# Optimization experiments

Hardware: AMD Instinct MI355X
Metric: run time of the kernel (lower is better)

The kernel has to match this reference:

```python
import jax, jax.numpy as jnp
import numpy as np

INPUT, HIDDEN = 40, 250
B, T = 256, 512


def lstm_layer(x_seq, W_ih, W_hh, b_ih, b_hh):
    """x_seq: [B,T,D_in] -> [B,T,H]. PyTorch gate order: i,f,g,o."""
    # Precompute input contribution with one big GEMM: [B,T,4H]
    xg = jnp.einsum('btd,gd->btg', x_seq, W_ih) + b_ih + b_hh
    xg_t = jnp.transpose(xg, (1, 0, 2))  # [T,B,4H]
    H = W_hh.shape[1]
    h0 = jnp.zeros((x_seq.shape[0], H), dtype=x_seq.dtype)
    c0 = jnp.zeros_like(h0)

    def step(carry, g_in):
        h, c = carry
        g = g_in + h @ W_hh.T  # [B,4H]
        i = jax.nn.sigmoid(g[:, :H])
        f = jax.nn.sigmoid(g[:, H:2 * H])
        gg = jnp.tanh(g[:, 2 * H:3 * H])
        o = jax.nn.sigmoid(g[:, 3 * H:])
        c = f * c + i * gg
        h = o * jnp.tanh(c)
        return (h, c), h

    _, hs = jax.lax.scan(step, (h0, c0), xg_t)  # hs: [T,B,H]
    return jnp.transpose(hs, (1, 0, 2))


def setup_inputs() -> dict:
    key = jax.random.key(0)
    ks = jax.random.split(key, 12)
    s_in = 1.0 / np.sqrt(HIDDEN)  # PyTorch LSTM init scale
    u = lambda k, shape: jax.random.uniform(k, shape, jnp.float32, -s_in, s_in)
    return {
        'x': jax.random.normal(ks[0], (B, T, INPUT), jnp.float32),
        'W_ih0': u(ks[1], (4 * HIDDEN, INPUT)),
        'W_hh0': u(ks[2], (4 * HIDDEN, HIDDEN)),
        'b_ih0': u(ks[3], (4 * HIDDEN,)),
        'b_hh0': u(ks[4], (4 * HIDDEN,)),
        'W_ih1': u(ks[5], (4 * HIDDEN, HIDDEN)),
        'W_hh1': u(ks[6], (4 * HIDDEN, HIDDEN)),
        'b_ih1': u(ks[7], (4 * HIDDEN,)),
        'b_hh1': u(ks[8], (4 * HIDDEN,)),
        'W_lin': u(ks[9], (1, HIDDEN)),
        'b_lin': u(ks[10], (1,)),
    }


def reference(x, W_ih0, W_hh0, b_ih0, b_hh0, W_ih1, W_hh1, b_ih1, b_hh1, W_lin, b_lin):
    h1 = lstm_layer(x, W_ih0, W_hh0, b_ih0, b_hh0)   # [B,T,H]
    h2 = lstm_layer(h1, W_ih1, W_hh1, b_ih1, b_hh1)  # [B,T,H]
    y = jnp.einsum('bth,oh->bto', h2, W_lin) + b_lin  # [B,T,1]
    return jax.nn.sigmoid(y)
```

## Files before the change

kernel.cpp:

```cpp
#include <hip/hip_runtime.h>
#include <cstdint>

#define B_TOT 256
#define T_LEN 512
#define NX    40
#define NH    250
#define HP    256
#define XP    64
#define K0    (XP + HP)
#define K1    (HP + HP)
#define MB    32
#define NU    16
#define NR    64
#define RING  8
#define LDSK  520
#define SLOTS 16
#define NFLAG (2 * 8 * 16 * SLOTS)
#define RSTEP (B_TOT * HP / 2)
#define XCD_AT(w) ((w) * SLOTS + 8)
#define BAR_IDX 9
#define GETREG_XCC 63508

typedef __attribute__((ext_vector_type(8))) short short8;
typedef __attribute__((ext_vector_type(4))) float float4v;

__device__ __forceinline__ unsigned short f2bf(float f) {
  unsigned u = __float_as_uint(f);
  u += 0x7FFFu + ((u >> 16) & 1u);
  return (unsigned short)(u >> 16);
}
__device__ __forceinline__ float bf2f(unsigned short h) {
  return __uint_as_float(((unsigned)h) << 16);
}
__device__ __forceinline__ float sigm(float x) { return 1.0f / (1.0f + __expf(-x)); }
__device__ __forceinline__ float tanh_f(float x) {
  float e = __expf(-2.0f * fabsf(x));
  float t = (1.0f - e) / (1.0f + e);
  return copysignf(t, x);
}
__device__ __forceinline__ unsigned ld_lic(const unsigned* p) {
  return __hip_atomic_load(p, __ATOMIC_RELAXED, __HIP_MEMORY_SCOPE_AGENT);
}
__device__ __forceinline__ void inv_l1() {
  asm volatile("buffer_inv\n\ts_waitcnt vmcnt(0)" ::: "memory");
  __builtin_amdgcn_sched_barrier(0);
}
template <bool FAST>
__device__ __forceinline__ unsigned ldh(const unsigned* p) {
  if (FAST) return *p;
  return ld_lic(p);
}
template <bool FAST>
__device__ __forceinline__ void sth(unsigned* p, unsigned v) {
  if (FAST) *p = v;
  else __hip_atomic_store(p, v, __ATOMIC_RELAXED, __HIP_MEMORY_SCOPE_AGENT);
}

template <int KSTEPS, int LAYER, bool FAST>
__device__ __forceinline__ void run_layer(
    int tid, int gg, int b0, int u0,
    const float* __restrict__ x, float* __restrict__ out, float blinv,
    unsigned short* __restrict__ h1bc, unsigned short* __restrict__ h2bc,
    int* __restrict__ c0s, int* __restrict__ c1s, int* __restrict__ mys,
    unsigned short (*WL)[LDSK], unsigned short (*inA)[LDSK],
    float (*gbuf)[NR + 4], float* biasS, float* wlinS) {
  const int lane = tid & 63, wv = tid >> 6;
  const int quad = lane >> 4, l15 = lane & 15;
  const int Mt = wv & 1, Np = wv >> 1;
  const int gb = b0 >> 5;
  const int irow = tid >> 3, icol = tid & 7;

  short8 bfrag[2][KSTEPS];
#pragma unroll
  for (int ks = 0; ks < KSTEPS; ++ks) {
#pragma unroll
    for (int i = 0; i < 2; ++i)
      bfrag[i][ks] = *(const short8*)&WL[Np * 32 + i * 16 + l15][ks * 32 + quad * 8];
  }

  float cA = 0.f, cB = 0.f;

#pragma unroll 1
  for (int t = 0; t < T_LEN; ++t) {
    if (wv == 0 && lane < 32) {
      const int* sl = ((lane < 16) ? c0s : c1s) + (lane & 15) * SLOTS;
      int thr;
      if (LAYER == 0) thr = (lane < 16) ? t : (t - RING + 1);
      else            thr = (lane < 16) ? (t + 1) : t;
      while (__hip_atomic_load(sl, __ATOMIC_RELAXED, __HIP_MEMORY_SCOPE_AGENT) < thr) {
        __builtin_amdgcn_s_sleep(1);
      }
    }
    __syncthreads();
    if (FAST && (LAYER == 1 || t > 0)) inv_l1();

    if (LAYER == 0) {
      if (t > 0) {
        const unsigned* s1 = (const unsigned*)h1bc +
            ((size_t)((t - 1) & (RING - 1)) * RSTEP + (size_t)gb * 4096);
        unsigned v[16];
#pragma unroll
        for (int k = 0; k < 16; ++k) v[k] = ldh<FAST>(s1 + tid + k * 256);
#pragma unroll
        for (int k = 0; k < 16; ++k)
          ((unsigned*)&inA[irow][0])[32 + k * 8 + icol] = v[k];
      }
      if (tid < 128) {
        int b = tid >> 2, c = tid & 3;
        const float* xp = x + ((size_t)(b0 + b) * T_LEN + (size_t)t) * NX + c * 10;
#pragma unroll
        for (int j = 0; j < 10; ++j) inA[b][c * 10 + j] = f2bf(xp[j]);
      }
    } else {
      const unsigned* s1 = (const unsigned*)h1bc +
          ((size_t)(t & (RING - 1)) * RSTEP + (size_t)gb * 4096);
      unsigned va[16], vb[16];
#pragma unroll
      for (int k = 0; k < 16; ++k) va[k] = ldh<FAST>(s1 + tid + k * 256);
      if (t > 0) {
        const unsigned* s2 = (const unsigned*)h2bc +
            ((size_t)((t - 1) & (RING - 1)) * RSTEP + (size_t)gb * 4096);
#pragma unroll
        for (int k = 0; k < 16; ++k) vb[k] = ldh<FAST>(s2 + tid + k * 256);
      }
#pragma unroll
      for (int k = 0; k < 16; ++k) {
        unsigned* row = (unsigned*)&inA[irow][0];
        row[k * 8 + icol] = va[k];
        if (t > 0) row[128 + k * 8 + icol] = vb[k];
      }
    }
    __syncthreads();

    float4v acc0 = {0.f, 0.f, 0.f, 0.f};
    float4v acc1 = {0.f, 0.f, 0.f, 0.f};
#pragma unroll
    for (int ks = 0; ks < KSTEPS; ++ks) {
      short8 a = *(const short8*)&inA[Mt * 16 + l15][ks * 32 + quad * 8];
      acc0 = __builtin_amdgcn_mfma_f32_16x16x32_bf16(a, bfrag[0][ks], acc0, 0, 0, 0);
      acc1 = __builtin_amdgcn_mfma_f32_16x16x32_bf16(a, bfrag[1][ks], acc1, 0, 0, 0);
    }
#pragma unroll
    for (int reg = 0; reg < 4; ++reg) {
      gbuf[Mt * 16 + quad * 4 + reg][Np * 32 + l15] = acc0[reg];
      gbuf[Mt * 16 + quad * 4 + reg][Np * 32 + 16 + l15] = acc1[reg];
    }
    __syncthreads();

    {
      int eb = tid >> 3, up = tid & 7;
      float4v ga = *(const float4v*)&gbuf[eb][up * 8];
      float4v gv = *(const float4v*)&gbuf[eb][up * 8 + 4];
      float iA = sigm(ga[0] + biasS[up * 8 + 0]);
      float fA = sigm(ga[1] + biasS[up * 8 + 1]);
      float gA = tanh_f(ga[2] + biasS[up * 8 + 2]);
      float oA = sigm(ga[3] + biasS[up * 8 + 3]);
      cA = fA * cA + iA * gA;
      float hA = oA * tanh_f(cA);
      float iB = sigm(gv[0] + biasS[up * 8 + 4]);
      float fB = sigm(gv[1] + biasS[up * 8 + 5]);
      float gB = tanh_f(gv[2] + biasS[up * 8 + 6]);
      float oB = sigm(gv[3] + biasS[up * 8 + 7]);
      cB = fB * cB + iB * gB;
      float hB = oB * tanh_f(cB);
      unsigned hv = (unsigned)f2bf(hA) | ((unsigned)f2bf(hB) << 16);
      unsigned* dst = (unsigned*)(LAYER ? h2bc : h1bc);
      size_t di = (size_t)(t & (RING - 1)) * RSTEP + (size_t)gb * 4096 +
                  (size_t)gg * 256 + tid;
      sth<FAST>(dst + di, hv);
    }

    __syncthreads();
    if (tid == 0)
      sth<FAST>((unsigned*)mys, (unsigned)(t + 1));

    if (LAYER == 1 && gg == 0 && t > 0) {
      int eb = tid >> 3, uc = tid & 7;
      float sum = 0.f;
#pragma unroll
      for (int j = 0; j < 4; ++j) {
        short8 hvv = *(const short8*)&inA[eb][HP + uc * 32 + j * 8];
#pragma unroll
        for (int e = 0; e < 8; ++e)
          sum += bf2f((unsigned short)hvv[e]) * wlinS[uc * 32 + j * 8 + e];
      }
      sum += __shfl_xor(sum, 1);
      sum += __shfl_xor(sum, 2);
      sum += __shfl_xor(sum, 4);
      if ((tid & 7) == 0)
        out[(size_t)(b0 + eb) * T_LEN + (t - 1)] = sigm(sum + blinv);
    }
  }

  if (LAYER == 1 && gg == 0) {
    if (wv == 0 && lane < 16) {
      const int* sl = c1s + lane * SLOTS;
      while (__hip_atomic_load(sl, __ATOMIC_RELAXED, __HIP_MEMORY_SCOPE_AGENT) < T_LEN) {
        __builtin_amdgcn_s_sleep(1);
      }
    }
    __syncthreads();
    if (FAST) inv_l1();
    int eb = tid >> 3, uc = tid & 7;
    const unsigned* base = (const unsigned*)h2bc +
        ((size_t)(511 & (RING - 1)) * RSTEP + (size_t)gb * 4096);
    float sum = 0.f;
#pragma unroll
    for (int g = 0; g < 2; ++g) {
      const unsigned* src = base + (size_t)(2 * uc + g) * 256 + eb * 8;
#pragma unroll
      for (int j = 0; j < 8; ++j) {
        unsigned dw = ldh<FAST>(src + j);
        sum += bf2f((unsigned short)(dw & 0xFFFFu)) * wlinS[uc * 32 + g * 16 + 2 * j];
        sum += bf2f((unsigned short)(dw >> 16)) * wlinS[uc * 32 + g * 16 + 2 * j + 1];
      }
    }
    sum += __shfl_xor(sum, 1);
    sum += __shfl_xor(sum, 2);
    sum += __shfl_xor(sum, 4);
    if ((tid & 7) == 0)
      out[(size_t)(b0 + eb) * T_LEN + 511] = sigm(sum + blinv);
  }
}

extern "C" __global__ void __launch_bounds__(256, 1) lstm_persist(
    const float* __restrict__ x,
    const float* __restrict__ Wih0, const float* __restrict__ Whh0,
    const float* __restrict__ bih0, const float* __restrict__ bhh0,
    const float* __restrict__ Wih1, const float* __restrict__ Whh1,
    const float* __restrict__ bih1, const float* __restrict__ bhh1,
    const float* __restrict__ Wlin, const float* __restrict__ blin,
    float* __restrict__ out,
    unsigned short* __restrict__ h1bc, unsigned short* __restrict__ h2bc,
    int* __restrict__ cnt) {
  __shared__ unsigned short WL[NR][LDSK];
  __shared__ unsigned short inA[MB][LDSK];
  __shared__ float gbuf[MB][NR + 4];
  __shared__ float biasS[NR];
  __shared__ float wlinS[HP];

  const int tid = threadIdx.x;
  const int wg = blockIdx.x;

  const unsigned xcc = ((unsigned)__builtin_amdgcn_s_getreg(GETREG_XCC)) & 15u;
  if (tid == 0) {
    __hip_atomic_store(cnt + XCD_AT(wg), (int)xcc, __ATOMIC_RELAXED,
                       __HIP_MEMORY_SCOPE_AGENT);
    __hip_atomic_fetch_add(cnt + BAR_IDX, 1, __ATOMIC_ACQ_REL,
                           __HIP_MEMORY_SCOPE_AGENT);
    while (__hip_atomic_load(cnt + BAR_IDX, __ATOMIC_ACQUIRE,
                             __HIP_MEMORY_SCOPE_AGENT) < 256)
      __builtin_amdgcn_s_sleep(8);
  }
  __syncthreads();
  int* sx = (int*)&gbuf[0][0];
  sx[tid] = __hip_atomic_load(cnt + XCD_AT(tid), __ATOMIC_RELAXED,
                              __HIP_MEMORY_SCOPE_AGENT);
  __syncthreads();
  const int myv = sx[wg];
  int rank = 0;
  unsigned long long hist = 0;
  bool ok = true;
  for (int j = 0; j < 256; ++j) {
    int v = sx[j];
    if ((unsigned)v > 7u) { ok = false; v = 0; }
    hist += 1ull << (v * 8);
    if (v == myv && j < wg) rank++;
  }
  ok = ok && (hist == 0x2020202020202020ull);
  __syncthreads();

  int layer, gb, gg;
  if (ok) { gb = myv;       layer = rank >> 4;    gg = rank & 15; }
  else    { layer = wg >> 7; gb = (wg >> 4) & 7;  gg = wg & 15;   }
  const int b0 = gb * MB, u0 = gg * NU;

  {
    const float* Wih = layer ? Wih1 : Wih0;
    const float* Whh = layer ? Whh1 : Whh0;
    const float* bi = layer ? bih1 : bih0;
    const float* bh = layer ? bhh1 : bhh0;
    const int K = layer ? K1 : K0;
    const int xw = layer ? NH : NX;
    const int xofs = layer ? HP : XP;
    int r = tid >> 2, c = tid & 3;
    int lu = r >> 2, g = r & 3, ug = u0 + lu;
    int row = g * NH + ug;
    int kq = K >> 2;
    for (int k = c * kq; k < (c + 1) * kq; ++k) {
      float v = 0.f;
      if (ug < NH) {
        if (k < xw) v = Wih[(size_t)row * xw + k];
        else if (k >= xofs && k < xofs + NH) v = Whh[(size_t)row * NH + (k - xofs)];
      }
      WL[r][k] = f2bf(v);
    }
    if (tid < NR) {
      int lu2 = tid >> 2, g2 = tid & 3, ug2 = u0 + lu2;
      biasS[tid] = (ug2 < NH) ? (bi[g2 * NH + ug2] + bh[g2 * NH + ug2]) : 0.f;
    }
    if (tid < HP) wlinS[tid] = (tid < NH) ? Wlin[tid] : 0.f;
    for (int i = tid; i < MB * LDSK; i += 256) ((unsigned short*)inA)[i] = 0;
  }
  __syncthreads();

  float blinv = blin[0];
  int* c0s = cnt + gb * 16 * SLOTS;
  int* c1s = cnt + (8 + gb) * 16 * SLOTS;
  int* mys = (layer ? c1s : c0s) + gg * SLOTS;

  if (ok) {
    if (layer == 0)
      run_layer<K0 / 32, 0, true>(tid, gg, b0, u0, x, out, blinv, h1bc, h2bc,
                                  c0s, c1s, mys, WL, inA, gbuf, biasS, wlinS);
    else
      run_layer<K1 / 32, 1, true>(tid, gg, b0, u0, x, out, blinv, h1bc, h2bc,
                                  c0s, c1s, mys, WL, inA, gbuf, biasS, wlinS);
  } else {
    if (layer == 0)
      run_layer<K0 / 32, 0, false>(tid, gg, b0, u0, x, out, blinv, h1bc, h2bc,
                                   c0s, c1s, mys, WL, inA, gbuf, biasS, wlinS);
    else
      run_layer<K1 / 32, 1, false>(tid, gg, b0, u0, x, out, blinv, h1bc, h2bc,
                                   c0s, c1s, mys, WL, inA, gbuf, biasS, wlinS);
  }
}

extern "C" __global__ void prep_zero(int* cnt) {
  int i = blockIdx.x * 256 + threadIdx.x;
  if (i < NFLAG)
    __hip_atomic_store(cnt + i, 0, __ATOMIC_RELAXED, __HIP_MEMORY_SCOPE_AGENT);
}

extern "C" void kernel_launch(void* const* d_in, const int* in_sizes, int n_in,
                              void* d_out, int out_size, void* d_ws, size_t ws_size,
                              hipStream_t stream) {
  const float* x    = (const float*)d_in[0];
  const float* Wih0 = (const float*)d_in[1];
  const float* Whh0 = (const float*)d_in[2];
  const float* bih0 = (const float*)d_in[3];
  const float* bhh0 = (const float*)d_in[4];
  const float* Wih1 = (const float*)d_in[5];
  const float* Whh1 = (const float*)d_in[6];
  const float* bih1 = (const float*)d_in[7];
  const float* bhh1 = (const float*)d_in[8];
  const float* Wlin = (const float*)d_in[9];
  const float* blin = (const float*)d_in[10];
  float* out = (float*)d_out;

  unsigned short* h1bc = (unsigned short*)d_ws;
  unsigned short* h2bc = h1bc + (size_t)RING * B_TOT * HP;
  int* cnt = (int*)((char*)d_ws + 2u * (size_t)RING * B_TOT * HP * sizeof(unsigned short));

  hipLaunchKernelGGL(prep_zero, dim3(16), dim3(256), 0, stream, cnt);

  void* args[] = {&x, &Wih0, &Whh0, &bih0, &bhh0, &Wih1, &Whh1, &bih1, &bhh1,
                  &Wlin, &blin, &out, &h1bc, &h2bc, &cnt};
  hipLaunchCooperativeKernel((void*)lstm_persist, dim3(256), dim3(256), args, 0u, stream);
}
```

Before: 1.251 ms.

## Prefetch x into registers, vectorize h exchange loads, spread output head across groups

Layer 0 now prefetches the next timestep's x inputs into registers after the barrier, so the global x load latency is hidden behind the MFMA and gate work. On the FAST path, the h-state exchange loads and LDS stores use 8-byte uint2 accesses instead of 4-byte ones, halving instruction count. The per-step linear-plus-sigmoid output head, previously done by all 256 threads in group 0, is split so each of the 16 groups computes two batch rows with 16 threads. This removes a serial tail from the critical workgroup, at the cost of a few extra registers and more duplicated code paths.

```diff
diff --git a/kernel.cpp b/kernel.cpp
--- a/kernel.cpp
+++ b/kernel.cpp
@@ -46,11 +46,6 @@
   __builtin_amdgcn_sched_barrier(0);
 }
 template <bool FAST>
-__device__ __forceinline__ unsigned ldh(const unsigned* p) {
-  if (FAST) return *p;
-  return ld_lic(p);
-}
-template <bool FAST>
 __device__ __forceinline__ void sth(unsigned* p, unsigned v) {
   if (FAST) *p = v;
   else __hip_atomic_store(p, v, __ATOMIC_RELAXED, __HIP_MEMORY_SCOPE_AGENT);
@@ -69,6 +64,7 @@
   const int Mt = wv & 1, Np = wv >> 1;
   const int gb = b0 >> 5;
   const int irow = tid >> 3, icol = tid & 7;
+  const int eb = tid >> 3, p8 = tid & 7, hi = p8 >> 2, q2 = 2 * (p8 & 3);
 
   short8 bfrag[2][KSTEPS];
 #pragma unroll
@@ -76,6 +72,14 @@
 #pragma unroll
     for (int i = 0; i < 2; ++i)
       bfrag[i][ks] = *(const short8*)&WL[Np * 32 + i * 16 + l15][ks * 32 + quad * 8];
+  }
+
+  float xr[10];
+  if (LAYER == 0 && tid < 128) {
+    int b = tid >> 2, c = tid & 3;
+    const float* xp0 = x + ((size_t)(b0 + b) * T_LEN + 0) * NX + c * 10;
+#pragma unroll
+    for (int j = 0; j < 10; ++j) xr[j] = xp0[j];
   }
 
   float cA = 0.f, cB = 0.f;
@@ -95,42 +99,88 @@
     if (FAST && (LAYER == 1 || t > 0)) inv_l1();
 
     if (LAYER == 0) {
-      if (t > 0) {
-        const unsigned* s1 = (const unsigned*)h1bc +
-            ((size_t)((t - 1) & (RING - 1)) * RSTEP + (size_t)gb * 4096);
-        unsigned v[16];
-#pragma unroll
-        for (int k = 0; k < 16; ++k) v[k] = ldh<FAST>(s1 + tid + k * 256);
-#pragma unroll
-        for (int k = 0; k < 16; ++k)
-          ((unsigned*)&inA[irow][0])[32 + k * 8 + icol] = v[k];
-      }
-      if (tid < 128) {
-        int b = tid >> 2, c = tid & 3;
-        const float* xp = x + ((size_t)(b0 + b) * T_LEN + (size_t)t) * NX + c * 10;
-#pragma unroll
-        for (int j = 0; j < 10; ++j) inA[b][c * 10 + j] = f2bf(xp[j]);
+      if (FAST) {
+        uint2 v[8];
+        if (t > 0) {
+          const unsigned* s1 = (const unsigned*)h1bc +
+              ((size_t)((t - 1) & (RING - 1)) * RSTEP + (size_t)gb * 4096);
+#pragma unroll
+          for (int k = 0; k < 8; ++k)
+            v[k] = *(const uint2*)(s1 + (8 * hi + k) * 256 + eb * 8 + q2);
+        }
+        if (tid < 128) {
+          int b = tid >> 2, c = tid & 3;
+#pragma unroll
+          for (int j = 0; j < 10; ++j) inA[b][c * 10 + j] = f2bf(xr[j]);
+        }
+        if (t > 0) {
+          unsigned* row = (unsigned*)&inA[eb][0];
+#pragma unroll
+          for (int k = 0; k < 8; ++k)
+            *(uint2*)&row[32 + (8 * hi + k) * 8 + q2] = v[k];
+        }
+      } else {
+        if (t > 0) {
+          const unsigned* s1 = (const unsigned*)h1bc +
+              ((size_t)((t - 1) & (RING - 1)) * RSTEP + (size_t)gb * 4096);
+          unsigned v[16];
+#pragma unroll
+          for (int k = 0; k < 16; ++k) v[k] = ld_lic(s1 + tid + k * 256);
+#pragma unroll
+          for (int k = 0; k < 16; ++k)
+            ((unsigned*)&inA[irow][0])[32 + k * 8 + icol] = v[k];
+        }
+        if (tid < 128) {
+          int b = tid >> 2, c = tid & 3;
+#pragma unroll
+          for (int j = 0; j < 10; ++j) inA[b][c * 10 + j] = f2bf(xr[j]);
+        }
       }
     } else {
       const unsigned* s1 = (const unsigned*)h1bc +
           ((size_t)(t & (RING - 1)) * RSTEP + (size_t)gb * 4096);
-      unsigned va[16], vb[16];
-#pragma unroll
-      for (int k = 0; k < 16; ++k) va[k] = ldh<FAST>(s1 + tid + k * 256);
-      if (t > 0) {
-        const unsigned* s2 = (const unsigned*)h2bc +
-            ((size_t)((t - 1) & (RING - 1)) * RSTEP + (size_t)gb * 4096);
-#pragma unroll
-        for (int k = 0; k < 16; ++k) vb[k] = ldh<FAST>(s2 + tid + k * 256);
-      }
-#pragma unroll
-      for (int k = 0; k < 16; ++k) {
-        unsigned* row = (unsigned*)&inA[irow][0];
-        row[k * 8 + icol] = va[k];
-        if (t > 0) row[128 + k * 8 + icol] = vb[k];
+      const unsigned* s2 = (const unsigned*)h2bc +
+          ((size_t)((t - 1) & (RING - 1)) * RSTEP + (size_t)gb * 4096);
+      if (FAST) {
+        uint2 va[8], vb[8];
+#pragma unroll
+        for (int k = 0; k < 8; ++k)
+          va[k] = *(const uint2*)(s1 + (8 * hi + k) * 256 + eb * 8 + q2);
+        if (t > 0) {
+#pragma unroll
+          for (int k = 0; k < 8; ++k)
+            vb[k] = *(const uint2*)(s2 + (8 * hi + k) * 256 + eb * 8 + q2);
+        }
+        unsigned* row = (unsigned*)&inA[eb][0];
+#pragma unroll
+        for (int k = 0; k < 8; ++k) {
+          *(uint2*)&row[(8 * hi + k) * 8 + q2] = va[k];
+          if (t > 0) *(uint2*)&row[128 + (8 * hi + k) * 8 + q2] = vb[k];
+        }
+      } else {
+        unsigned va[16], vb[16];
+#pragma unroll
+        for (int k = 0; k < 16; ++k) va[k] = ld_lic(s1 + tid + k * 256);
+        if (t > 0) {
+#pragma unroll
+          for (int k = 0; k < 16; ++k) vb[k] = ld_lic(s2 + tid + k * 256);
+        }
+#pragma unroll
+        for (int k = 0; k < 16; ++k) {
+          unsigned* row = (unsigned*)&inA[irow][0];
+          row[k * 8 + icol] = va[k];
+          if (t > 0) row[128 + k * 8 + icol] = vb[k];
+        }
       }
     }
     __syncthreads();
+
+    if (LAYER == 0 && tid < 128 && t + 1 < T_LEN) {
+      int b = tid >> 2, c = tid & 3;
+      const float* xp = x + ((size_t)(b0 + b) * T_LEN + (size_t)(t + 1)) * NX + c * 10;
+#pragma unroll
+      for (int j = 0; j < 10; ++j) xr[j] = xp[j];
+    }
 
     float4v acc0 = {0.f, 0.f, 0.f, 0.f};
     float4v acc1 = {0.f, 0.f, 0.f, 0.f};
@@ -148,9 +198,9 @@
     __syncthreads();
 
     {
-      int eb = tid >> 3, up = tid & 7;
-      float4v ga = *(const float4v*)&gbuf[eb][up * 8];
-      float4v gv = *(const float4v*)&gbuf[eb][up * 8 + 4];
+      int ebg = tid >> 3, up = tid & 7;
+      float4v ga = *(const float4v*)&gbuf[ebg][up * 8];
+      float4v gv = *(const float4v*)&gbuf[ebg][up * 8 + 4];
       float iA = sigm(ga[0] + biasS[up * 8 + 0]);
       float fA = sigm(ga[1] + biasS[up * 8 + 1]);
       float gA = tanh_f(ga[2] + biasS[up * 8 + 2]);
@@ -174,12 +224,12 @@
     if (tid == 0)
       sth<FAST>((unsigned*)mys, (unsigned)(t + 1));
 
-    if (LAYER == 1 && gg == 0 && t > 0) {
-      int eb = tid >> 3, uc = tid & 7;
+    if (LAYER == 1 && t > 0 && tid < 16) {
+      int eb2 = 2 * gg + (tid >> 3), uc = tid & 7;
       float sum = 0.f;
 #pragma unroll
       for (int j = 0; j < 4; ++j) {
-        short8 hvv = *(const short8*)&inA[eb][HP + uc * 32 + j * 8];
+        short8 hvv = *(const short8*)&inA[eb2][HP + uc * 32 + j * 8];
 #pragma unroll
         for (int e = 0; e < 8; ++e)
           sum += bf2f((unsigned short)hvv[e]) * wlinS[uc * 32 + j * 8 + e];
@@ -188,11 +238,11 @@
       sum += __shfl_xor(sum, 2);
       sum += __shfl_xor(sum, 4);
       if ((tid & 7) == 0)
-        out[(size_t)(b0 + eb) * T_LEN + (t - 1)] = sigm(sum + blinv);
-    }
-  }
-
-  if (LAYER == 1 && gg == 0) {
+        out[(size_t)(b0 + eb2) * T_LEN + (t - 1)] = sigm(sum + blinv);
+    }
+  }
+
+  if (LAYER == 1) {
     if (wv == 0 && lane < 16) {
       const int* sl = c1s + lane * SLOTS;
       while (__hip_atomic_load(sl, __ATOMIC_RELAXED, __HIP_MEMORY_SCOPE_AGENT) < T_LEN) {
@@ -201,25 +251,27 @@
     }
     __syncthreads();
     if (FAST) inv_l1();
-    int eb = tid >> 3, uc = tid & 7;
-    const unsigned* base = (const unsigned*)h2bc +
-        ((size_t)(511 & (RING - 1)) * RSTEP + (size_t)gb * 4096);
-    float sum = 0.f;
-#pragma unroll
-    for (int g = 0; g < 2; ++g) {
-      const unsigned* src = base + (size_t)(2 * uc + g) * 256 + eb * 8;
-#pragma unroll
-      for (int j = 0; j < 8; ++j) {
-        unsigned dw = ldh<FAST>(src + j);
-        sum += bf2f((unsigned short)(dw & 0xFFFFu)) * wlinS[uc * 32 + g * 16 + 2 * j];
-        sum += bf2f((unsigned short)(dw >> 16)) * wlinS[uc * 32 + g * 16 + 2 * j + 1];
-      }
-    }
-    sum += __shfl_xor(sum, 1);
-    sum += __shfl_xor(sum, 2);
-    sum += __shfl_xor(sum, 4);
-    if ((tid & 7) == 0)
-      out[(size_t)(b0 + eb) * T_LEN + 511] = sigm(sum + blinv);
+    if (tid < 16) {
+      int eb2 = 2 * gg + (tid >> 3), uc = tid & 7;
+      const unsigned* base = (const unsigned*)h2bc +
+          ((size_t)(511 & (RING - 1)) * RSTEP + (size_t)gb * 4096);
+      float sum = 0.f;
+#pragma unroll
+      for (int g = 0; g < 2; ++g) {
+        const unsigned* src = base + (size_t)(2 * uc + g) * 256 + eb2 * 8;
+#pragma unroll
+        for (int j = 0; j < 8; ++j) {
+          unsigned dw = FAST ? src[j] : ld_lic(src + j);
+          sum += bf2f((unsigned short)(dw & 0xFFFFu)) * wlinS[uc * 32 + g * 16 + 2 * j];
+          sum += bf2f((unsigned short)(dw >> 16)) * wlinS[uc * 32 + g * 16 + 2 * j + 1];
+        }
+      }
+      sum += __shfl_xor(sum, 1);
+      sum += __shfl_xor(sum, 2);
+      sum += __shfl_xor(sum, 4);
+      if ((tid & 7) == 0)
+        out[(size_t)(b0 + eb2) * T_LEN + 511] = sigm(sum + blinv);
+    }
   }
 }
 
```

Result: slower. 1.344 ms (+7.5%).

## Prefetch next-step x into registers, cache bias, spread output projection across blocks

Applied to the files above, without the earlier changes.

Loads the layer-0 input slice for step t+1 into registers during the current step, so the global x load latency overlaps with the MFMA and gate work instead of sitting on the recurrent critical path. Keeps the per-thread gate biases in registers rather than re-reading them from shared memory each step. Spreads the final linear/sigmoid projection across all 16 layer-1 blocks of a batch group, each handling two batch rows with 16 threads, instead of having the gg==0 block compute all 32 rows. This takes serial output work off a single block, which the layer-0 blocks may wait on, at the cost of some extra registers.

```diff
diff --git a/kernel.cpp b/kernel.cpp
--- a/kernel.cpp
+++ b/kernel.cpp
@@ -78,6 +78,18 @@
       bfrag[i][ks] = *(const short8*)&WL[Np * 32 + i * 16 + l15][ks * 32 + quad * 8];
   }
 
+  float bloc[8];
+#pragma unroll
+  for (int i = 0; i < 8; ++i) bloc[i] = biasS[(tid & 7) * 8 + i];
+
+  float xr[10];
+  if (LAYER == 0 && tid < 128) {
+    int b = tid >> 2, c = tid & 3;
+    const float* xp0 = x + ((size_t)(b0 + b) * T_LEN + 0) * NX + c * 10;
+#pragma unroll
+    for (int j = 0; j < 10; ++j) xr[j] = xp0[j];
+  }
+
   float cA = 0.f, cB = 0.f;
 
 #pragma unroll 1
@@ -107,9 +119,8 @@
       }
       if (tid < 128) {
         int b = tid >> 2, c = tid & 3;
-        const float* xp = x + ((size_t)(b0 + b) * T_LEN + (size_t)t) * NX + c * 10;
-#pragma unroll
-        for (int j = 0; j < 10; ++j) inA[b][c * 10 + j] = f2bf(xp[j]);
+#pragma unroll
+        for (int j = 0; j < 10; ++j) inA[b][c * 10 + j] = f2bf(xr[j]);
       }
     } else {
       const unsigned* s1 = (const unsigned*)h1bc +
@@ -132,6 +143,13 @@
     }
     __syncthreads();
 
+    if (LAYER == 0 && tid < 128 && t + 1 < T_LEN) {
+      int b = tid >> 2, c = tid & 3;
+      const float* xp = x + ((size_t)(b0 + b) * T_LEN + (size_t)(t + 1)) * NX + c * 10;
+#pragma unroll
+      for (int j = 0; j < 10; ++j) xr[j] = xp[j];
+    }
+
     float4v acc0 = {0.f, 0.f, 0.f, 0.f};
     float4v acc1 = {0.f, 0.f, 0.f, 0.f};
 #pragma unroll
@@ -148,19 +166,19 @@
     __syncthreads();
 
     {
-      int eb = tid >> 3, up = tid & 7;
-      float4v ga = *(const float4v*)&gbuf[eb][up * 8];
-      float4v gv = *(const float4v*)&gbuf[eb][up * 8 + 4];
-      float iA = sigm(ga[0] + biasS[up * 8 + 0]);
-      float fA = sigm(ga[1] + biasS[up * 8 + 1]);
-      float gA = tanh_f(ga[2] + biasS[up * 8 + 2]);
-      float oA = sigm(ga[3] + biasS[up * 8 + 3]);
+      int ebg = tid >> 3;
+      float4v ga = *(const float4v*)&gbuf[ebg][(tid & 7) * 8];
+      float4v gv = *(const float4v*)&gbuf[ebg][(tid & 7) * 8 + 4];
+      float iA = sigm(ga[0] + bloc[0]);
+      float fA = sigm(ga[1] + bloc[1]);
+      float gA = tanh_f(ga[2] + bloc[2]);
+      float oA = sigm(ga[3] + bloc[3]);
       cA = fA * cA + iA * gA;
       float hA = oA * tanh_f(cA);
-      float iB = sigm(gv[0] + biasS[up * 8 + 4]);
-      float fB = sigm(gv[1] + biasS[up * 8 + 5]);
-      float gB = tanh_f(gv[2] + biasS[up * 8 + 6]);
-      float oB = sigm(gv[3] + biasS[up * 8 + 7]);
+      float iB = sigm(gv[0] + bloc[4]);
+      float fB = sigm(gv[1] + bloc[5]);
+      float gB = tanh_f(gv[2] + bloc[6]);
+      float oB = sigm(gv[3] + bloc[7]);
       cB = fB * cB + iB * gB;
       float hB = oB * tanh_f(cB);
       unsigned hv = (unsigned)f2bf(hA) | ((unsigned)f2bf(hB) << 16);
@@ -174,12 +192,12 @@
     if (tid == 0)
       sth<FAST>((unsigned*)mys, (unsigned)(t + 1));
 
-    if (LAYER == 1 && gg == 0 && t > 0) {
-      int eb = tid >> 3, uc = tid & 7;
+    if (LAYER == 1 && t > 0 && tid < 16) {
+      int eb2 = 2 * gg + (tid >> 3), uc = tid & 7;
       float sum = 0.f;
 #pragma unroll
       for (int j = 0; j < 4; ++j) {
-        short8 hvv = *(const short8*)&inA[eb][HP + uc * 32 + j * 8];
+        short8 hvv = *(const short8*)&inA[eb2][HP + uc * 32 + j * 8];
 #pragma unroll
         for (int e = 0; e < 8; ++e)
           sum += bf2f((unsigned short)hvv[e]) * wlinS[uc * 32 + j * 8 + e];
@@ -188,11 +206,11 @@
       sum += __shfl_xor(sum, 2);
       sum += __shfl_xor(sum, 4);
       if ((tid & 7) == 0)
-        out[(size_t)(b0 + eb) * T_LEN + (t - 1)] = sigm(sum + blinv);
-    }
-  }
-
-  if (LAYER == 1 && gg == 0) {
+        out[(size_t)(b0 + eb2) * T_LEN + (t - 1)] = sigm(sum + blinv);
+    }
+  }
+
+  if (LAYER == 1) {
     if (wv == 0 && lane < 16) {
       const int* sl = c1s + lane * SLOTS;
       while (__hip_atomic_load(sl, __ATOMIC_RELAXED, __HIP_MEMORY_SCOPE_AGENT) < T_LEN) {
@@ -201,25 +219,27 @@
     }
     __syncthreads();
     if (FAST) inv_l1();
-    int eb = tid >> 3, uc = tid & 7;
-    const unsigned* base = (const unsigned*)h2bc +
-        ((size_t)(511 & (RING - 1)) * RSTEP + (size_t)gb * 4096);
-    float sum = 0.f;
-#pragma unroll
-    for (int g = 0; g < 2; ++g) {
-      const unsigned* src = base + (size_t)(2 * uc + g) * 256 + eb * 8;
-#pragma unroll
-      for (int j = 0; j < 8; ++j) {
-        unsigned dw = ldh<FAST>(src + j);
-        sum += bf2f((unsigned short)(dw & 0xFFFFu)) * wlinS[uc * 32 + g * 16 + 2 * j];
-        sum += bf2f((unsigned short)(dw >> 16)) * wlinS[uc * 32 + g * 16 + 2 * j + 1];
-      }
-    }
-    sum += __shfl_xor(sum, 1);
-    sum += __shfl_xor(sum, 2);
-    sum += __shfl_xor(sum, 4);
-    if ((tid & 7) == 0)
-      out[(size_t)(b0 + eb) * T_LEN + 511] = sigm(sum + blinv);
+    if (tid < 16) {
+      int eb2 = 2 * gg + (tid >> 3), uc = tid & 7;
+      const unsigned* base = (const unsigned*)h2bc +
+          ((size_t)(511 & (RING - 1)) * RSTEP + (size_t)gb * 4096);
+      float sum = 0.f;
+#pragma unroll
+      for (int g = 0; g < 2; ++g) {
+        const unsigned* src = base + (size_t)(2 * uc + g) * 256 + eb2 * 8;
+#pragma unroll
+        for (int j = 0; j < 8; ++j) {
+          unsigned dw = ldh<FAST>(src + j);
+          sum += bf2f((unsigned short)(dw & 0xFFFFu)) * wlinS[uc * 32 + g * 16 + 2 * j];
+          sum += bf2f((unsigned short)(dw >> 16)) * wlinS[uc * 32 + g * 16 + 2 * j + 1];
+        }
+      }
+      sum += __shfl_xor(sum, 1);
+      sum += __shfl_xor(sum, 2);
+      sum += __shfl_xor(sum, 4);
+      if ((tid & 7) == 0)
+        out[(size_t)(b0 + eb2) * T_LEN + 511] = sigm(sum + blinv);
+    }
   }
 }
 
```

After: 1.217 ms. -2.8%, faster.
